# Optimization experiments

Measured on AMD Instinct MI355X. Metric: run time of the kernel, lower is better.

Reference implementation:

```python
import jax, jax.numpy as jnp
import numpy as np

ALPHA = 0.1


def setup_inputs() -> dict:
    key = jax.random.key(0)
    kx, ky = jax.random.split(key)
    x = jax.random.normal(kx, (8192, 64), dtype=jnp.float32)
    y = jax.random.normal(ky, (8192, 64), dtype=jnp.float32)
    return {"x": x, "y": y}


def reference(x, y):
    # Gram matrices [N, N]
    xx = x @ x.T
    yy = y @ y.T
    xy = x @ y.T
    rx = jnp.diagonal(xx)[None, :]  # [1, N] row of squared norms of x
    ry = jnp.diagonal(yy)[None, :]  # [1, N]
    # Gaussian kernel matrices; rx.T + rx - 2*xx == pairwise sq. distances
    K = jnp.exp(-ALPHA * (rx.T + rx - 2.0 * xx))
    L = jnp.exp(-ALPHA * (ry.T + ry - 2.0 * yy))
    P = jnp.exp(-ALPHA * (rx.T + ry - 2.0 * xy))
    return K.sum() + L.sum() - 2.0 * P.sum()
```

## Files before the change

### kernel.cpp

```cpp
#include <hip/hip_runtime.h>

#define ALPHA 0.1f
#define LOG2E 1.4426950408889634f
#define NJ 4

typedef __attribute__((ext_vector_type(8))) short bf16x8;
typedef __attribute__((ext_vector_type(4))) float f32x4;

__device__ __forceinline__ unsigned int f2bf(float f) {
    unsigned int u = __float_as_uint(f);
    return (u + 0x7FFFu + ((u >> 16) & 1u)) >> 16;
}

__global__ void mmd_zero(float* out) { out[0] = 0.f; }

__global__ __launch_bounds__(256) void mmd_prep(const float* __restrict__ x,
                                                const float* __restrict__ y,
                                                uint4* __restrict__ z4,
                                                float* __restrict__ bias,
                                                float* __restrict__ out, int N) {
    int t = blockIdx.x * 256 + threadIdx.x;
    if (t == 0) out[0] = 0.f;
    int row = t >> 3, kc = t & 7;
    const float4* src = (row < N) ? (const float4*)x : (const float4*)y;
    int r = (row < N) ? row : row - N;
    float4 a = src[r * 16 + kc * 2];
    float4 b = src[r * 16 + kc * 2 + 1];
    unsigned int w0 = f2bf(a.x), w1 = f2bf(a.y), w2 = f2bf(a.z), w3 = f2bf(a.w);
    unsigned int w4 = f2bf(b.x), w5 = f2bf(b.y), w6 = f2bf(b.z), w7 = f2bf(b.w);
    uint4 pk;
    pk.x = w0 | (w1 << 16);
    pk.y = w2 | (w3 << 16);
    pk.z = w4 | (w5 << 16);
    pk.w = w6 | (w7 << 16);
    int tile = row >> 7, rr = row & 127;
    z4[tile * 1024 + kc * 128 + rr] = pk;

    float s = 0.f;
    unsigned int ws[8] = {w0, w1, w2, w3, w4, w5, w6, w7};
#pragma unroll
    for (int i = 0; i < 8; ++i) {
        float v = __uint_as_float(ws[i] << 16);
        s = fmaf(v, v, s);
    }
    s += __shfl_xor(s, 1);
    s += __shfl_xor(s, 2);
    s += __shfl_xor(s, 4);
    if (kc == 0) bias[row] = -ALPHA * LOG2E * s;
}

__global__ __launch_bounds__(256, 4) void mmd_main4(const uint4* __restrict__ z4,
                                                    const float* __restrict__ bias,
                                                    float* __restrict__ out,
                                                    int T2, int TX) {
    __shared__ float ldsRed[4];

    int u = blockIdx.x, bi = 0;
    int per = (T2 + NJ - 1) / NJ;
    while (u >= per) { u -= per; ++bi; per = (T2 - bi + NJ - 1) / NJ; }
    int j0 = bi + u * NJ;
    int nj = min(NJ, T2 - j0);

    int tid = threadIdx.x;
    int w = tid >> 6, l = tid & 63;
    int wr = w >> 1, wc = w & 1;
    int lrow = l & 15, lk = l >> 4;

    const uint4* gA = z4 + bi * 1024;
    bf16x8 af[4][2];
#pragma unroll
    for (int mb = 0; mb < 4; ++mb)
#pragma unroll
        for (int kh = 0; kh < 2; ++kh)
            af[mb][kh] = *(const bf16x8*)(gA + (kh * 4 + lk) * 128 +
                                          wr * 64 + mb * 16 + lrow);
    float bA[4][4];
#pragma unroll
    for (int mb = 0; mb < 4; ++mb)
#pragma unroll
        for (int q = 0; q < 4; ++q)
            bA[mb][q] = bias[bi * 128 + wr * 64 + mb * 16 + lk * 4 + q];

    const float C2 = 2.f * ALPHA * LOG2E;
    float stot = 0.f;

    for (int j = 0; j < nj; ++j) {
        int bj = j0 + j;
        const uint4* gB = z4 + bj * 1024;
        const float* biasB = bias + bj * 128 + wc * 64 + lrow;
        float sp[4] = {0.f, 0.f, 0.f, 0.f};

#pragma unroll
        for (int h = 0; h < 2; ++h) {
            bf16x8 bfr[2][2];
#pragma unroll
            for (int nb = 0; nb < 2; ++nb)
#pragma unroll
                for (int kh = 0; kh < 2; ++kh)
                    bfr[nb][kh] = *(const bf16x8*)(gB + (kh * 4 + lk) * 128 +
                                                   wc * 64 + (h * 2 + nb) * 16 + lrow);
            float ebB[2];
#pragma unroll
            for (int nb = 0; nb < 2; ++nb)
                ebB[nb] = __builtin_amdgcn_exp2f(biasB[(h * 2 + nb) * 16]);

            f32x4 acc[4][2];
#pragma unroll
            for (int mb = 0; mb < 4; ++mb)
#pragma unroll
                for (int nb = 0; nb < 2; ++nb)
                    acc[mb][nb] = (f32x4){0.f, 0.f, 0.f, 0.f};

#pragma unroll
            for (int mb = 0; mb < 4; ++mb) {
#pragma unroll
                for (int nb = 0; nb < 2; ++nb) {
                    acc[mb][nb] = __builtin_amdgcn_mfma_f32_16x16x32_bf16(
                        af[mb][0], bfr[nb][0], acc[mb][nb], 0, 0, 0);
                    acc[mb][nb] = __builtin_amdgcn_mfma_f32_16x16x32_bf16(
                        af[mb][1], bfr[nb][1], acc[mb][nb], 0, 0, 0);
                }
            }

#pragma unroll
            for (int mb = 0; mb < 4; ++mb)
#pragma unroll
                for (int nb = 0; nb < 2; ++nb)
#pragma unroll
                    for (int q = 0; q < 4; ++q) {
                        float e = __builtin_amdgcn_exp2f(
                            fmaf(C2, acc[mb][nb][q], bA[mb][q]));
                        sp[q] = fmaf(ebB[nb], e, sp[q]);
                    }
        }

        float wgt = ((bj == bi) ? 1.f : 2.f) *
                    (((bi < TX) != (bj < TX)) ? -1.f : 1.f);
        stot = fmaf(wgt, (sp[0] + sp[1]) + (sp[2] + sp[3]), stot);
    }

#pragma unroll
    for (int off = 32; off > 0; off >>= 1)
        stot += __shfl_down(stot, off, 64);
    if (l == 0) ldsRed[w] = stot;
    __syncthreads();
    if (tid == 0)
        atomicAdd(out, ldsRed[0] + ldsRed[1] + ldsRed[2] + ldsRed[3]);
}

__global__ __launch_bounds__(256) void mmd_main(const float* __restrict__ x,
                                                const float* __restrict__ y,
                                                float* __restrict__ out, int T) {
    __shared__ uint4 ldsT[4][1024];
    __shared__ float ldsB[4][128];
    __shared__ float ldsRed[4];

    int u = blockIdx.x, bi = 0, rem = T;
    while (u >= rem) { u -= rem; ++bi; --rem; }
    int bj = bi + u;
    bool diag = (bi == bj);

    int tid = threadIdx.x;
    int RI = bi * 128, RJ = bj * 128;

    const float4* x4 = (const float4*)x;
    const float4* y4 = (const float4*)y;
#pragma unroll
    for (int p = 0; p < 16; ++p) {
        int task = p * 256 + tid;
        int buf = task >> 10;
        int q = task & 1023;
        int row = q >> 3, kc = q & 7;
        int base = (buf & 1) ? RJ : RI;
        const float4* src = (buf < 2) ? x4 : y4;
        float4 a = src[(base + row) * 16 + kc * 2];
        float4 b = src[(base + row) * 16 + kc * 2 + 1];
        uint4 pk;
        pk.x = f2bf(a.x) | (f2bf(a.y) << 16);
        pk.y = f2bf(a.z) | (f2bf(a.w) << 16);
        pk.z = f2bf(b.x) | (f2bf(b.y) << 16);
        pk.w = f2bf(b.z) | (f2bf(b.w) << 16);
        ldsT[buf][kc * 128 + row] = pk;
    }
    __syncthreads();

#pragma unroll
    for (int p = 0; p < 2; ++p) {
        int task = p * 256 + tid;
        int buf = task >> 7, row = task & 127;
        float s = 0.f;
#pragma unroll
        for (int kc = 0; kc < 8; ++kc) {
            uint4 v = ldsT[buf][kc * 128 + row];
            unsigned int wds[4] = {v.x, v.y, v.z, v.w};
#pragma unroll
            for (int i = 0; i < 4; ++i) {
                float lo = __uint_as_float(wds[i] << 16);
                float hi = __uint_as_float(wds[i] & 0xFFFF0000u);
                s = fmaf(lo, lo, s);
                s = fmaf(hi, hi, s);
            }
        }
        ldsB[buf][row] = -ALPHA * LOG2E * s;
    }
    __syncthreads();

    int w = tid >> 6, l = tid & 63;
    int wr = w >> 1, wc = w & 1;
    int lrow = l & 15, lk = l >> 4;

    const int aBufs[4] = {0, 2, 0, 1};
    const int bBufs[4] = {1, 3, 3, 2};
    float wKL = diag ? 1.f : 2.f;
    const float wts[4] = {wKL, wKL, -2.f, -2.f};
    int npass = diag ? 3 : 4;

    const float C2 = 2.f * ALPHA * LOG2E;
    float stot = 0.f;

    for (int ps = 0; ps < npass; ++ps) {
        int ab = aBufs[ps], bb = bBufs[ps];
        bf16x8 af[4][2], bfr[4][2];
#pragma unroll
        for (int mb = 0; mb < 4; ++mb) {
#pragma unroll
            for (int kh = 0; kh < 2; ++kh) {
                int ar = wr * 64 + mb * 16 + lrow;
                int br = wc * 64 + mb * 16 + lrow;
                int kc = kh * 4 + lk;
                af[mb][kh]  = *(const bf16x8*)&ldsT[ab][kc * 128 + ar];
                bfr[mb][kh] = *(const bf16x8*)&ldsT[bb][kc * 128 + br];
            }
        }
        f32x4 acc[4][4];
#pragma unroll
        for (int mb = 0; mb < 4; ++mb)
#pragma unroll
            for (int nb = 0; nb < 4; ++nb)
                acc[mb][nb] = (f32x4){0.f, 0.f, 0.f, 0.f};
#pragma unroll
        for (int mb = 0; mb < 4; ++mb) {
#pragma unroll
            for (int nb = 0; nb < 4; ++nb) {
                acc[mb][nb] = __builtin_amdgcn_mfma_f32_16x16x32_bf16(
                    af[mb][0], bfr[nb][0], acc[mb][nb], 0, 0, 0);
                acc[mb][nb] = __builtin_amdgcn_mfma_f32_16x16x32_bf16(
                    af[mb][1], bfr[nb][1], acc[mb][nb], 0, 0, 0);
            }
        }
        float bA[4][4], bB[4];
#pragma unroll
        for (int mb = 0; mb < 4; ++mb)
#pragma unroll
            for (int q = 0; q < 4; ++q)
                bA[mb][q] = ldsB[ab][wr * 64 + mb * 16 + lk * 4 + q];
#pragma unroll
        for (int nb = 0; nb < 4; ++nb)
            bB[nb] = ldsB[bb][wc * 64 + nb * 16 + lrow];
        float sp = 0.f;
#pragma unroll
        for (int mb = 0; mb < 4; ++mb) {
#pragma unroll
            for (int nb = 0; nb < 4; ++nb) {
#pragma unroll
                for (int q = 0; q < 4; ++q) {
                    float arg = fmaf(C2, acc[mb][nb][q], bA[mb][q] + bB[nb]);
                    sp += __builtin_amdgcn_exp2f(arg);
                }
            }
        }
        stot = fmaf(wts[ps], sp, stot);
    }

#pragma unroll
    for (int off = 32; off > 0; off >>= 1)
        stot += __shfl_down(stot, off, 64);
    if (l == 0) ldsRed[w] = stot;
    __syncthreads();
    if (tid == 0)
        atomicAdd(out, ldsRed[0] + ldsRed[1] + ldsRed[2] + ldsRed[3]);
}

extern "C" void kernel_launch(void* const* d_in, const int* in_sizes, int n_in,
                              void* d_out, int out_size, void* d_ws, size_t ws_size,
                              hipStream_t stream) {
    (void)n_in; (void)out_size;
    const float* x = (const float*)d_in[0];
    const float* y = (const float*)d_in[1];
    float* out = (float*)d_out;

    int N = in_sizes[0] / 64;
    size_t zBytes = (size_t)2 * N * 128;
    size_t need = zBytes + (size_t)2 * N * 4;

    if (ws_size >= need) {
        uint4* z4 = (uint4*)d_ws;
        float* bias = (float*)((char*)d_ws + zBytes);
        int T2 = (2 * N) / 128;
        int TX = N / 128;
        int prepBlocks = (2 * N * 8) / 256;
        int mainBlocks = 0;
        for (int bi = 0; bi < T2; ++bi) mainBlocks += (T2 - bi + NJ - 1) / NJ;
        hipLaunchKernelGGL(mmd_prep, dim3(prepBlocks), dim3(256), 0, stream,
                           x, y, z4, bias, out, N);
        hipLaunchKernelGGL(mmd_main4, dim3(mainBlocks), dim3(256), 0, stream,
                           z4, bias, out, T2, TX);
    } else {
        int T = N / 128;
        int nblocks = T * (T + 1) / 2;
        hipLaunchKernelGGL(mmd_zero, dim3(1), dim3(1), 0, stream, out);
        hipLaunchKernelGGL(mmd_main, dim3(nblocks), dim3(256), 0, stream,
                           x, y, out, T);
    }
}
```

Measured before the change: 44.23 us.

## Offload part of exp2 to FMA polynomial and replace float atomics with last-block reduction

For 6 of the 16 accumulator elements per 4x4 group, exp2 is computed with a cubic polynomial plus ldexp on the FMA pipe instead of the transcendental unit. The goal is to balance work between the transcendental and FMA ALUs, which are the bottleneck in the epilogue. Per-block partial sums are written to a buffer, and the last block to finish, found with an atomic counter, reduces them. This replaces the contended float atomicAdd on one output and makes the result deterministic. The polynomial approximation adds some error, roughly 1e-4 relative.

```diff
diff --git a/kernel.cpp b/kernel.cpp
--- a/kernel.cpp
+++ b/kernel.cpp
@@ -18,9 +18,9 @@
                                                 const float* __restrict__ y,
                                                 uint4* __restrict__ z4,
                                                 float* __restrict__ bias,
-                                                float* __restrict__ out, int N) {
+                                                int* __restrict__ counter, int N) {
     int t = blockIdx.x * 256 + threadIdx.x;
-    if (t == 0) out[0] = 0.f;
+    if (t == 0) *counter = 0;
     int row = t >> 3, kc = t & 7;
     const float4* src = (row < N) ? (const float4*)x : (const float4*)y;
     int r = (row < N) ? row : row - N;
@@ -49,11 +49,14 @@
     if (kc == 0) bias[row] = -ALPHA * LOG2E * s;
 }
 
-__global__ __launch_bounds__(256, 4) void mmd_main4(const uint4* __restrict__ z4,
+__global__ __launch_bounds__(256, 4) void mmd_main5(const uint4* __restrict__ z4,
                                                     const float* __restrict__ bias,
+                                                    float* __restrict__ part,
+                                                    int* __restrict__ counter,
                                                     float* __restrict__ out,
-                                                    int T2, int TX) {
+                                                    int T2, int TX, int nBlocks) {
     __shared__ float ldsRed[4];
+    __shared__ int lastFlag;
 
     int u = blockIdx.x, bi = 0;
     int per = (T2 + NJ - 1) / NJ;
@@ -99,10 +102,12 @@
                 for (int kh = 0; kh < 2; ++kh)
                     bfr[nb][kh] = *(const bf16x8*)(gB + (kh * 4 + lk) * 128 +
                                                    wc * 64 + (h * 2 + nb) * 16 + lrow);
-            float ebB[2];
-#pragma unroll
-            for (int nb = 0; nb < 2; ++nb)
-                ebB[nb] = __builtin_amdgcn_exp2f(biasB[(h * 2 + nb) * 16]);
+            float bBr[2], ebB[2];
+#pragma unroll
+            for (int nb = 0; nb < 2; ++nb) {
+                bBr[nb] = biasB[(h * 2 + nb) * 16];
+                ebB[nb] = __builtin_amdgcn_exp2f(bBr[nb]);
+            }
 
             f32x4 acc[4][2];
 #pragma unroll
@@ -123,15 +128,27 @@
             }
 
 #pragma unroll
-            for (int mb = 0; mb < 4; ++mb)
-#pragma unroll
-                for (int nb = 0; nb < 2; ++nb)
+            for (int mb = 0; mb < 4; ++mb) {
+#pragma unroll
+                for (int nb = 0; nb < 2; ++nb) {
 #pragma unroll
                     for (int q = 0; q < 4; ++q) {
-                        float e = __builtin_amdgcn_exp2f(
-                            fmaf(C2, acc[mb][nb][q], bA[mb][q]));
-                        sp[q] = fmaf(ebB[nb], e, sp[q]);
+                        float arg = fmaf(C2, acc[mb][nb][q], bA[mb][q]);
+                        if (mb * 4 + q < 10) {
+                            float e = __builtin_amdgcn_exp2f(arg);
+                            sp[q] = fmaf(ebB[nb], e, sp[q]);
+                        } else {
+                            float a2 = arg + bBr[nb];
+                            float fl = floorf(a2);
+                            float f  = a2 - fl;
+                            float p  = fmaf(f, 0.07800543f, 0.22606716f);
+                            p = fmaf(f, p, 0.69583354f);
+                            p = fmaf(f, p, 0.99992520f);
+                            sp[q] += ldexpf(p, (int)fl);
+                        }
                     }
+                }
+            }
         }
 
         float wgt = ((bj == bi) ? 1.f : 2.f) *
@@ -144,8 +161,25 @@
         stot += __shfl_down(stot, off, 64);
     if (l == 0) ldsRed[w] = stot;
     __syncthreads();
-    if (tid == 0)
-        atomicAdd(out, ldsRed[0] + ldsRed[1] + ldsRed[2] + ldsRed[3]);
+    if (tid == 0) {
+        part[blockIdx.x] = ldsRed[0] + ldsRed[1] + ldsRed[2] + ldsRed[3];
+        __threadfence();
+        int old = atomicAdd(counter, 1);
+        lastFlag = (old == nBlocks - 1) ? 1 : 0;
+    }
+    __syncthreads();
+    if (lastFlag) {
+        __threadfence();
+        float s = 0.f;
+        for (int i = tid; i < nBlocks; i += 256) s += part[i];
+#pragma unroll
+        for (int off = 32; off > 0; off >>= 1)
+            s += __shfl_down(s, off, 64);
+        if (l == 0) ldsRed[w] = s;
+        __syncthreads();
+        if (tid == 0)
+            out[0] = ldsRed[0] + ldsRed[1] + ldsRed[2] + ldsRed[3];
+    }
 }
 
 __global__ __launch_bounds__(256) void mmd_main(const float* __restrict__ x,
@@ -290,21 +324,26 @@
     float* out = (float*)d_out;
 
     int N = in_sizes[0] / 64;
+    int T2 = (2 * N) / 128;
+    int TX = N / 128;
+    int mainBlocks = 0;
+    for (int bi = 0; bi < T2; ++bi) mainBlocks += (T2 - bi + NJ - 1) / NJ;
+
     size_t zBytes = (size_t)2 * N * 128;
-    size_t need = zBytes + (size_t)2 * N * 4;
+    size_t bBytes = (size_t)2 * N * 4;
+    size_t pBytes = (size_t)mainBlocks * 4;
+    size_t need = zBytes + bBytes + pBytes + 4;
 
     if (ws_size >= need) {
         uint4* z4 = (uint4*)d_ws;
         float* bias = (float*)((char*)d_ws + zBytes);
-        int T2 = (2 * N) / 128;
-        int TX = N / 128;
+        float* part = (float*)((char*)d_ws + zBytes + bBytes);
+        int* counter = (int*)((char*)d_ws + zBytes + bBytes + pBytes);
         int prepBlocks = (2 * N * 8) / 256;
-        int mainBlocks = 0;
-        for (int bi = 0; bi < T2; ++bi) mainBlocks += (T2 - bi + NJ - 1) / NJ;
         hipLaunchKernelGGL(mmd_prep, dim3(prepBlocks), dim3(256), 0, stream,
-                           x, y, z4, bias, out, N);
-        hipLaunchKernelGGL(mmd_main4, dim3(mainBlocks), dim3(256), 0, stream,
-                           z4, bias, out, T2, TX);
+                           x, y, z4, bias, counter, N);
+        hipLaunchKernelGGL(mmd_main5, dim3(mainBlocks), dim3(256), 0, stream,
+                           z4, bias, part, counter, out, T2, TX, mainBlocks);
     } else {
         int T = N / 128;
         int nblocks = T * (T + 1) / 2;
```

New measurement: 69.45 us. 1.57x slower.
